# Kernel optimization log

Hardware: AMD Instinct MI355X
Metric: run time of the kernel (lower is better)

The kernel has to match this reference:

```python
import jax, jax.numpy as jnp
import numpy as np

# footprints from the module: RB = 8-neighbor ring (center excluded), G = 4-neighbor cross
RB_OFFSETS = [(-1, -1), (-1, 0), (-1, 1), (0, -1), (0, 1), (1, -1), (1, 0), (1, 1)]
G_OFFSETS = [(-1, 0), (0, -1), (0, 1), (1, 0)]
N_ITER = 3


def _footprint_median(x, offsets):
    """scipy.ndimage.median_filter with a boolean footprint.
    scipy uses rank = n//2 of the sorted footprint values (no averaging for even n)
    and 'reflect' boundary mode (== numpy 'symmetric' padding).
    x: [B, H, W]
    """
    B, H, W = x.shape
    xp = jnp.pad(x, ((0, 0), (1, 1), (1, 1)), mode='symmetric')
    vals = jnp.stack([xp[:, 1 + dy:1 + dy + H, 1 + dx:1 + dx + W]
                      for dy, dx in offsets], axis=0)  # [n, B, H, W]
    n = len(offsets)
    return jnp.sort(vals, axis=0)[n // 2]


def _conv3(x, k):
    """3x3 conv with symmetric padding. x: [B,H,W], k: [3,3] -> [B,H,W]."""
    xp = jnp.pad(x, ((0, 0), (1, 1), (1, 1)), mode='symmetric')[:, None]  # [B,1,H+2,W+2]
    kern = k[None, None].astype(x.dtype)  # [1,1,3,3]
    out = jax.lax.conv_general_dilated(xp, kern, (1, 1), 'VALID')
    return out[:, 0]


def _demosaick(x):
    """Naive bilinear demosaick of a GRBG Bayer mosaic. x: [B,H,W] -> [B,3,H,W]."""
    B, H, W = x.shape
    yy, xx = jnp.meshgrid(jnp.arange(H), jnp.arange(W), indexing='ij')
    r_mask = ((yy % 2 == 0) & (xx % 2 == 1)).astype(x.dtype)
    b_mask = ((yy % 2 == 1) & (xx % 2 == 0)).astype(x.dtype)
    g_mask = 1.0 - r_mask - b_mask
    KG = jnp.array([[0., 1., 0.], [1., 4., 1.], [0., 1., 0.]]) / 4.0
    KRB = jnp.array([[1., 2., 1.], [2., 4., 2.], [1., 2., 1.]]) / 4.0
    R = _conv3(x * r_mask, KRB)
    G = _conv3(x * g_mask, KG)
    Bc = _conv3(x * b_mask, KRB)
    return jnp.stack([R, G, Bc], axis=1)


def reference(image):
    # image: [B, 1, H, W] Bayer mosaic
    d = _demosaick(image[:, 0])  # [B, 3, H, W]
    R, G, B = d[:, 0], d[:, 1], d[:, 2]
    for _ in range(N_ITER):
        # medians are non-differentiable in the original (numpy roundtrip)
        R = jax.lax.stop_gradient(_footprint_median(R - G, RB_OFFSETS)) + G
        B = jax.lax.stop_gradient(_footprint_median(B - G, RB_OFFSETS)) + G
        G = 0.5 * (jax.lax.stop_gradient(_footprint_median(G - R, G_OFFSETS))
                   + jax.lax.stop_gradient(_footprint_median(G - B, G_OFFSETS))
                   + R + B)
    return jnp.stack([R, G, B], axis=1)


def setup_inputs() -> dict:
    key = jax.random.key(0)
    image = jax.random.uniform(key, (8, 1, 1024, 1024), dtype=jnp.float32)
    return {"image": image}
```

## Files before the change

kernel.cpp:

```cpp
#include <hip/hip_runtime.h>

#define HH 1024
#define WW 1024
#define NB 8
constexpr int PLANE = HH * WW;

#define S   84
#define RG  46
#define NTHR 512

typedef _Float16 h2 __attribute__((ext_vector_type(2)));

__device__ __forceinline__ int clampi(int v, int lo, int hi) {
    return v < lo ? lo : (v > hi ? hi : v);
}

union U2H { unsigned u; h2 h; };
__device__ __forceinline__ h2 u2h(unsigned v) { U2H x; x.u = v; return x.h; }
__device__ __forceinline__ unsigned h2u(h2 h) { U2H x; x.h = h; return x.u; }
__device__ __forceinline__ unsigned packdiff(float a, float b) {
    h2 h; h.x = (_Float16)a; h.y = (_Float16)b; return h2u(h);
}
__device__ __forceinline__ h2 swap16(h2 x) {
    unsigned u = h2u(x);
    return u2h(__builtin_amdgcn_alignbit(u, u, 16));
}

__device__ __forceinline__ void cswap2(h2& a, h2& b) {
    h2 lo = __builtin_elementwise_min(a, b);
    b = __builtin_elementwise_max(a, b);
    a = lo;
}

__device__ __forceinline__ h2 med8p(h2 v0, h2 v1, h2 v2, h2 v3,
                                    h2 v4, h2 v5, h2 v6, h2 v7) {
    cswap2(v0, v1); cswap2(v2, v3); cswap2(v4, v5); cswap2(v6, v7);
    cswap2(v0, v2); cswap2(v1, v3); cswap2(v4, v6); cswap2(v5, v7);
    cswap2(v1, v2); cswap2(v5, v6);
    h2 p2 = __builtin_elementwise_min(v2, v6), p3 = __builtin_elementwise_min(v3, v7);
    h2 p4 = __builtin_elementwise_max(v0, v4), p5 = __builtin_elementwise_max(v1, v5);
    return __builtin_elementwise_max(__builtin_elementwise_min(p3, p5),
                                     __builtin_elementwise_max(p2, p4));
}

__device__ __forceinline__ h2 med4p(h2 a, h2 b, h2 c, h2 d) {
    h2 ab_hi = __builtin_elementwise_max(a, b), ab_lo = __builtin_elementwise_min(a, b);
    h2 cd_hi = __builtin_elementwise_max(c, d), cd_lo = __builtin_elementwise_min(c, d);
    return __builtin_elementwise_max(__builtin_elementwise_min(ab_hi, cd_hi),
                                     __builtin_elementwise_max(ab_lo, cd_lo));
}

__device__ __forceinline__ void demo_acc(float v, int pyn, int pxn, int ady, int adx,
                                         float& accR, float& accG, float& accB) {
    bool isr = (pyn == 0) && (pxn == 1);
    bool isb = (pyn == 1) && (pxn == 0);
    float wrb = 0.25f * (float)((2 - ady) * (2 - adx));
    int man = ady + adx;
    float wg = (man == 0) ? 1.0f : ((man == 1) ? 0.25f : 0.0f);
    accR += isr ? wrb * v : 0.0f;
    accB += isb ? wrb * v : 0.0f;
    accG += (!isr && !isb) ? wg * v : 0.0f;
}

template <int CA>
__device__ __forceinline__ void load4u(const unsigned* row, int c0, unsigned w[4]) {
    if constexpr (CA == 0) {
        uint4 q = *reinterpret_cast<const uint4*>(row + c0);
        w[0] = q.x; w[1] = q.y; w[2] = q.z; w[3] = q.w;
    } else {
        uint2 a = *reinterpret_cast<const uint2*>(row + c0);
        uint2 b = *reinterpret_cast<const uint2*>(row + c0 + 2);
        w[0] = a.x; w[1] = a.y; w[2] = b.x; w[3] = b.y;
    }
}
template <int CA>
__device__ __forceinline__ void load6u(const unsigned* row, int c0, unsigned w[6]) {
    if constexpr (CA == 0) {
        uint4 q = *reinterpret_cast<const uint4*>(row + c0);
        w[0] = row[c0 - 1];
        w[1] = q.x; w[2] = q.y; w[3] = q.z; w[4] = q.w;
        w[5] = row[c0 + 4];
    } else {
        uint4 a = *reinterpret_cast<const uint4*>(row + c0 - 2);
        uint4 b = *reinterpret_cast<const uint4*>(row + c0 + 2);
        w[0] = a.y; w[1] = a.z; w[2] = a.w; w[3] = b.x; w[4] = b.y; w[5] = b.z;
    }
}
template <int CA>
__device__ __forceinline__ void store4u(unsigned* row, int c0, const unsigned v[4]) {
    if constexpr (CA == 0) {
        *reinterpret_cast<uint4*>(row + c0) = make_uint4(v[0], v[1], v[2], v[3]);
    } else {
        *reinterpret_cast<uint2*>(row + c0) = make_uint2(v[0], v[1]);
        *reinterpret_cast<uint2*>(row + c0 + 2) = make_uint2(v[2], v[3]);
    }
}

template <int R0, int NRP, int C0, int NG>
__device__ __forceinline__ void p1_int(const unsigned* __restrict__ sdRB,
                                       unsigned* __restrict__ uRB, int tid) {
    static_assert((C0 & 3) == 2, "p1_int needs C0 % 4 == 2");
    if (tid < NRP * NG) {
        int rp = tid / NG, g = tid - rp * NG;
        int r0 = R0 + 2 * rp;
        int c0 = C0 + 4 * g;
        int B = c0 - 2;
        unsigned w[4][6];
#pragma unroll
        for (int i = 0; i < 4; ++i) {
            const unsigned* row = &sdRB[(r0 - 1 + i) * S + B];
            uint4 q0 = *reinterpret_cast<const uint4*>(row);
            uint4 q1 = *reinterpret_cast<const uint4*>(row + 4);
            w[i][0] = q0.y; w[i][1] = q0.z; w[i][2] = q0.w;
            w[i][3] = q1.x; w[i][4] = q1.y; w[i][5] = q1.z;
        }
#pragma unroll
        for (int rr = 0; rr < 2; ++rr) {
            unsigned rv[4];
#pragma unroll
            for (int i = 0; i < 4; ++i) {
                h2 m = med8p(u2h(w[rr][i]), u2h(w[rr][i + 1]), u2h(w[rr][i + 2]),
                             u2h(w[rr + 1][i]), u2h(w[rr + 1][i + 2]),
                             u2h(w[rr + 2][i]), u2h(w[rr + 2][i + 1]), u2h(w[rr + 2][i + 2]));
                rv[i] = h2u(-m);
            }
            store4u<2>(&uRB[(r0 + rr) * S], c0, rv);
        }
    }
}

template <int R0, int NRP, int C0, int NG, int CA, bool FINAL>
__device__ __forceinline__ void p2_int(_Float16* __restrict__ sG, unsigned* __restrict__ sdRB,
                                       const unsigned* __restrict__ uRB, int tid,
                                       int y0, int x0,
                                       float* __restrict__ oR, float* __restrict__ oG,
                                       float* __restrict__ oB) {
    if (tid < NRP * NG) {
        int rp = tid / NG, g = tid - rp * NG;
        int r0 = R0 + 2 * rp;
        int c0 = C0 + 4 * g;
        unsigned wm[4], wp[4], w0[6], w1[6];
        load4u<CA>(&uRB[(r0 - 1) * S], c0, wm);
        load6u<CA>(&uRB[(r0) * S], c0, w0);
        load6u<CA>(&uRB[(r0 + 1) * S], c0, w1);
        load4u<CA>(&uRB[(r0 + 2) * S], c0, wp);
        h2 ga0 = *reinterpret_cast<const h2*>(&sG[r0 * S + c0]);
        h2 ga1 = *reinterpret_cast<const h2*>(&sG[r0 * S + c0 + 2]);
        h2 gb0 = *reinterpret_cast<const h2*>(&sG[(r0 + 1) * S + c0]);
        h2 gb1 = *reinterpret_cast<const h2*>(&sG[(r0 + 1) * S + c0 + 2]);
        _Float16 gr0[4] = {ga0.x, ga0.y, ga1.x, ga1.y};
        _Float16 gr1[4] = {gb0.x, gb0.y, gb1.x, gb1.y};
        const h2 half2v = {(_Float16)0.5f, (_Float16)0.5f};

        unsigned nd0[4], nd1[4];
        float R4[2][4], G4[2][4], B4[2][4];
#pragma unroll
        for (int i = 0; i < 4; ++i) {
            {
                h2 m = med4p(u2h(wm[i]), u2h(w0[i]), u2h(w0[i + 2]), u2h(w1[i + 1]));
                h2 uc = u2h(w0[i + 1]);
                h2 gg; gg.x = gr0[i]; gg.y = gr0[i];
                h2 RB = gg - uc;
                h2 Gn2 = ((m + swap16(m)) + (RB + swap16(RB))) * half2v;
                if constexpr (FINAL) {
                    R4[0][i] = (float)RB.x; B4[0][i] = (float)RB.y; G4[0][i] = (float)Gn2.x;
                } else {
                    nd0[i] = h2u(RB - Gn2);
                    gr0[i] = Gn2.x;
                }
            }
            {
                h2 m = med4p(u2h(w0[i + 1]), u2h(w1[i]), u2h(w1[i + 2]), u2h(wp[i]));
                h2 uc = u2h(w1[i + 1]);
                h2 gg; gg.x = gr1[i]; gg.y = gr1[i];
                h2 RB = gg - uc;
                h2 Gn2 = ((m + swap16(m)) + (RB + swap16(RB))) * half2v;
                if constexpr (FINAL) {
                    R4[1][i] = (float)RB.x; B4[1][i] = (float)RB.y; G4[1][i] = (float)Gn2.x;
                } else {
                    nd1[i] = h2u(RB - Gn2);
                    gr1[i] = Gn2.x;
                }
            }
        }
        if constexpr (FINAL) {
#pragma unroll
            for (int rr = 0; rr < 2; ++rr) {
                size_t o = (size_t)(y0 + r0 + rr) * WW + (x0 + c0);
                *reinterpret_cast<float4*>(&oR[o]) = make_float4(R4[rr][0], R4[rr][1], R4[rr][2], R4[rr][3]);
                *reinterpret_cast<float4*>(&oG[o]) = make_float4(G4[rr][0], G4[rr][1], G4[rr][2], G4[rr][3]);
                *reinterpret_cast<float4*>(&oB[o]) = make_float4(B4[rr][0], B4[rr][1], B4[rr][2], B4[rr][3]);
            }
        } else {
            h2 s00; s00.x = gr0[0]; s00.y = gr0[1];
            h2 s01; s01.x = gr0[2]; s01.y = gr0[3];
            h2 s10; s10.x = gr1[0]; s10.y = gr1[1];
            h2 s11; s11.x = gr1[2]; s11.y = gr1[3];
            *reinterpret_cast<h2*>(&sG[r0 * S + c0]) = s00;
            *reinterpret_cast<h2*>(&sG[r0 * S + c0 + 2]) = s01;
            *reinterpret_cast<h2*>(&sG[(r0 + 1) * S + c0]) = s10;
            *reinterpret_cast<h2*>(&sG[(r0 + 1) * S + c0 + 2]) = s11;
            store4u<CA>(&sdRB[r0 * S], c0, nd0);
            store4u<CA>(&sdRB[(r0 + 1) * S], c0, nd1);
        }
    }
}

__device__ void p1_b(const unsigned* sdRB, unsigned* uRB, int tid,
                     int y0, int x0, int rlo, int nr, int clo, int nc) {
    for (int t = tid; t < nr * nc; t += NTHR) {
        int r = rlo + t / nc, c = clo + t - (t / nc) * nc;
        int gy = clampi(y0 + r, 0, HH - 1), gx = clampi(x0 + c, 0, WW - 1);
        int rm = clampi(gy - 1, 0, HH - 1) - y0, rp = clampi(gy + 1, 0, HH - 1) - y0;
        int cm = clampi(gx - 1, 0, WW - 1) - x0, cp = clampi(gx + 1, 0, WW - 1) - x0;
        h2 m = med8p(u2h(sdRB[rm * S + cm]), u2h(sdRB[rm * S + c]), u2h(sdRB[rm * S + cp]),
                     u2h(sdRB[r * S + cm]), u2h(sdRB[r * S + cp]),
                     u2h(sdRB[rp * S + cm]), u2h(sdRB[rp * S + c]), u2h(sdRB[rp * S + cp]));
        uRB[r * S + c] = h2u(-m);
    }
}

__device__ void p2_b(_Float16* sG, unsigned* sdRB, const unsigned* uRB, int tid,
                     int y0, int x0, int rlo, int nr, int clo, int nc, bool fin,
                     float* oR, float* oG, float* oB) {
    for (int t = tid; t < nr * nc; t += NTHR) {
        int r = rlo + t / nc, c = clo + t - (t / nc) * nc;
        int gy = clampi(y0 + r, 0, HH - 1), gx = clampi(x0 + c, 0, WW - 1);
        int rm = clampi(gy - 1, 0, HH - 1) - y0, rp = clampi(gy + 1, 0, HH - 1) - y0;
        int cm = clampi(gx - 1, 0, WW - 1) - x0, cp = clampi(gx + 1, 0, WW - 1) - x0;
        h2 m = med4p(u2h(uRB[rm * S + c]), u2h(uRB[r * S + cm]),
                     u2h(uRB[r * S + cp]), u2h(uRB[rp * S + c]));
        h2 uc = u2h(uRB[r * S + c]);
        float Gc = (float)sG[r * S + c];
        float Rn = Gc - (float)uc.x, Bn = Gc - (float)uc.y;
        float Gn = 0.5f * ((float)m.x + (float)m.y + Rn + Bn);
        if (fin) {
            size_t o = (size_t)(y0 + r) * WW + (x0 + c);
            oR[o] = Rn; oG[o] = Gn; oB[o] = Bn;
        } else {
            sG[r * S + c] = (_Float16)Gn;
            sdRB[r * S + c] = packdiff(Rn - Gn, Bn - Gn);
        }
    }
}

__global__ __launch_bounds__(512, 8) void fused_kernel(const float* __restrict__ img,
                                                       float* __restrict__ dst) {
    __shared__ __align__(16) unsigned smem[9660];
    unsigned* uRB = smem;
    unsigned* sdRB = smem + RG * S;
    _Float16* sG = reinterpret_cast<_Float16*>(smem + 2 * RG * S);
    float* sI = reinterpret_cast<float*>(smem);

    int bx = blockIdx.x, by = blockIdx.y, bb = blockIdx.z;
    int x0 = bx * 64 - 8, y0 = by * 32 - 7;
    const float* im = img + (size_t)bb * PLANE;
    float* oR = dst + (size_t)bb * 3 * PLANE;
    float* oG = oR + PLANE;
    float* oB = oR + 2 * PLANE;
    int tid = threadIdx.x;
    bool interior = (bx >= 1 && bx <= 14 && by >= 1 && by <= 30);

    if (interior) {
        if (tid < 22 * 19) {
            int qi = tid / 19, g = tid - (tid / 19) * 19;
            int rA = 1 + 2 * qi;
            int B = 4 * g;
            const float* base = im + (size_t)(y0 + rA - 1) * WW + (x0 + B);
            float w[4][6];
#pragma unroll
            for (int i = 0; i < 4; ++i) {
                float4 a = *reinterpret_cast<const float4*>(base + (size_t)i * WW);
                float4 b = *reinterpret_cast<const float4*>(base + (size_t)i * WW + 4);
                w[i][0] = a.y; w[i][1] = a.z; w[i][2] = a.w;
                w[i][3] = b.x; w[i][4] = b.y; w[i][5] = b.z;
            }
#pragma unroll
            for (int q = 0; q < 2; ++q) {
                int jb = 1 + 2 * q;
                float g00 = w[1][jb];
                float r00 = 0.5f * (w[1][jb - 1] + w[1][jb + 1]);
                float b00 = 0.5f * (w[0][jb] + w[2][jb]);
                float r01 = w[1][jb + 1];
                float g01 = 0.25f * (w[0][jb + 1] + w[2][jb + 1] + w[1][jb] + w[1][jb + 2]);
                float b01 = 0.25f * (w[0][jb] + w[0][jb + 2] + w[2][jb] + w[2][jb + 2]);
                float b10 = w[2][jb];
                float g10 = 0.25f * (w[1][jb] + w[3][jb] + w[2][jb - 1] + w[2][jb + 1]);
                float r10 = 0.25f * (w[1][jb - 1] + w[1][jb + 1] + w[3][jb - 1] + w[3][jb + 1]);
                float g11 = w[2][jb + 1];
                float r11 = 0.5f * (w[1][jb + 1] + w[3][jb + 1]);
                float b11 = 0.5f * (w[2][jb] + w[2][jb + 2]);
                int a0 = rA * S + 2 + 4 * g + 2 * q;
                h2 gh0; gh0.x = (_Float16)g00; gh0.y = (_Float16)g01;
                h2 gh1; gh1.x = (_Float16)g10; gh1.y = (_Float16)g11;
                *reinterpret_cast<h2*>(&sG[a0]) = gh0;
                *reinterpret_cast<h2*>(&sG[a0 + S]) = gh1;
                *reinterpret_cast<uint2*>(&sdRB[a0]) =
                    make_uint2(packdiff(r00 - g00, b00 - g00), packdiff(r01 - g01, b01 - g01));
                *reinterpret_cast<uint2*>(&sdRB[a0 + S]) =
                    make_uint2(packdiff(r10 - g10, b10 - g10), packdiff(r11 - g11, b11 - g11));
            }
        }
        __syncthreads();
        p1_int<2, 21, 2, 19>(sdRB, uRB, tid);
        __syncthreads();
        p2_int<3, 20, 4, 18, 0, false>(sG, sdRB, uRB, tid, y0, x0, oR, oG, oB);
        __syncthreads();
        p1_int<4, 19, 2, 19>(sdRB, uRB, tid);
        __syncthreads();
        p2_int<5, 18, 6, 17, 2, false>(sG, sdRB, uRB, tid, y0, x0, oR, oG, oB);
        __syncthreads();
        p1_int<6, 17, 6, 17>(sdRB, uRB, tid);
        __syncthreads();
        p2_int<7, 16, 8, 16, 0, true>(sG, sdRB, uRB, tid, y0, x0, oR, oG, oB);
    } else {
        for (int t = tid; t < RG * S; t += NTHR) {
            int r = t / S, c = t - (t / S) * S;
            int gy = clampi(y0 + r, 0, HH - 1), gx = clampi(x0 + c, 0, WW - 1);
            sI[r * S + c] = im[(size_t)gy * WW + gx];
        }
        __syncthreads();
        {
            for (int t = tid; t < 44 * 76; t += NTHR) {
                int r = 1 + t / 76, c = 2 + t - (t / 76) * 76;
                int gy = clampi(y0 + r, 0, HH - 1), gx = clampi(x0 + c, 0, WW - 1);
                float accR = 0.f, accG = 0.f, accB = 0.f;
#pragma unroll
                for (int dy = -1; dy <= 1; ++dy)
#pragma unroll
                    for (int dx = -1; dx <= 1; ++dx) {
                        int cy = clampi(gy + dy, 0, HH - 1);
                        int cx = clampi(gx + dx, 0, WW - 1);
                        float v = sI[(cy - y0) * S + (cx - x0)];
                        demo_acc(v, cy & 1, cx & 1, dy < 0 ? -dy : dy, dx < 0 ? -dx : dx,
                                 accR, accG, accB);
                    }
                sG[r * S + c] = (_Float16)accG;
                sdRB[r * S + c] = packdiff(accR - accG, accB - accG);
            }
        }
        __syncthreads();
        p1_b(sdRB, uRB, tid, y0, x0, 2, 42, 3, 74);
        __syncthreads();
        p2_b(sG, sdRB, uRB, tid, y0, x0, 3, 40, 4, 72, false, oR, oG, oB);
        __syncthreads();
        p1_b(sdRB, uRB, tid, y0, x0, 4, 38, 5, 70);
        __syncthreads();
        p2_b(sG, sdRB, uRB, tid, y0, x0, 5, 36, 6, 68, false, oR, oG, oB);
        __syncthreads();
        p1_b(sdRB, uRB, tid, y0, x0, 6, 34, 7, 66);
        __syncthreads();
        p2_b(sG, sdRB, uRB, tid, y0, x0, 7, 32, 8, 64, true, oR, oG, oB);
    }
}

extern "C" void kernel_launch(void* const* d_in, const int* in_sizes, int n_in,
                              void* d_out, int out_size, void* d_ws, size_t ws_size,
                              hipStream_t stream) {
    const float* img = (const float*)d_in[0];
    float* out = (float*)d_out;
    dim3 block(NTHR);
    dim3 grid(16, 32, NB);
    fused_kernel<<<grid, block, 0, stream>>>(img, out);
}
```

Measured before the change: 136.3 us.

## Reuse vectorized interior paths for boundary tiles via halo refresh copies

Boundary tiles no longer use the scalar clamped-index median passes. They run the same templated vectorized p1_int/p2_int passes as interior tiles, with extra refresh steps that copy in-image values into out-of-image halo cells to emulate symmetric reflection. The demosaick for boundary tiles also uses the quad-vectorized path for the in-image core, falling back to the per-pixel clamped version only for the remaining edge pixels. This removes the divergence and slow path of edge blocks at the cost of extra sync barriers and correctness subtleties in the halo emulation. The p2_int final output writes for out-of-image cells also need care.

```diff
diff --git a/kernel.cpp b/kernel.cpp
--- a/kernel.cpp
+++ b/kernel.cpp
@@ -60,6 +60,35 @@
     accR += isr ? wrb * v : 0.0f;
     accB += isb ? wrb * v : 0.0f;
     accG += (!isr && !isb) ? wg * v : 0.0f;
+}
+
+__device__ __forceinline__ void demo_quads2(const float w[4][6], unsigned* __restrict__ sdRB,
+                                            _Float16* __restrict__ sG, int a0base) {
+#pragma unroll
+    for (int q = 0; q < 2; ++q) {
+        int jb = 1 + 2 * q;
+        float g00 = w[1][jb];
+        float r00 = 0.5f * (w[1][jb - 1] + w[1][jb + 1]);
+        float b00 = 0.5f * (w[0][jb] + w[2][jb]);
+        float r01 = w[1][jb + 1];
+        float g01 = 0.25f * (w[0][jb + 1] + w[2][jb + 1] + w[1][jb] + w[1][jb + 2]);
+        float b01 = 0.25f * (w[0][jb] + w[0][jb + 2] + w[2][jb] + w[2][jb + 2]);
+        float b10 = w[2][jb];
+        float g10 = 0.25f * (w[1][jb] + w[3][jb] + w[2][jb - 1] + w[2][jb + 1]);
+        float r10 = 0.25f * (w[1][jb - 1] + w[1][jb + 1] + w[3][jb - 1] + w[3][jb + 1]);
+        float g11 = w[2][jb + 1];
+        float r11 = 0.5f * (w[1][jb + 1] + w[3][jb + 1]);
+        float b11 = 0.5f * (w[2][jb] + w[2][jb + 2]);
+        int a0 = a0base + 2 * q;
+        h2 gh0; gh0.x = (_Float16)g00; gh0.y = (_Float16)g01;
+        h2 gh1; gh1.x = (_Float16)g10; gh1.y = (_Float16)g11;
+        *reinterpret_cast<h2*>(&sG[a0]) = gh0;
+        *reinterpret_cast<h2*>(&sG[a0 + S]) = gh1;
+        *reinterpret_cast<uint2*>(&sdRB[a0]) =
+            make_uint2(packdiff(r00 - g00, b00 - g00), packdiff(r01 - g01, b01 - g01));
+        *reinterpret_cast<uint2*>(&sdRB[a0 + S]) =
+            make_uint2(packdiff(r10 - g10, b10 - g10), packdiff(r11 - g11, b11 - g11));
+    }
 }
 
 template <int CA>
@@ -206,41 +235,27 @@
     }
 }
 
-__device__ void p1_b(const unsigned* sdRB, unsigned* uRB, int tid,
-                     int y0, int x0, int rlo, int nr, int clo, int nc) {
+__device__ __forceinline__ void refresh_d(unsigned* __restrict__ sdRB, _Float16* __restrict__ sG,
+                                          int tid, int y0, int x0,
+                                          int rlo, int nr, int clo, int nc) {
     for (int t = tid; t < nr * nc; t += NTHR) {
         int r = rlo + t / nc, c = clo + t - (t / nc) * nc;
-        int gy = clampi(y0 + r, 0, HH - 1), gx = clampi(x0 + c, 0, WW - 1);
-        int rm = clampi(gy - 1, 0, HH - 1) - y0, rp = clampi(gy + 1, 0, HH - 1) - y0;
-        int cm = clampi(gx - 1, 0, WW - 1) - x0, cp = clampi(gx + 1, 0, WW - 1) - x0;
-        h2 m = med8p(u2h(sdRB[rm * S + cm]), u2h(sdRB[rm * S + c]), u2h(sdRB[rm * S + cp]),
-                     u2h(sdRB[r * S + cm]), u2h(sdRB[r * S + cp]),
-                     u2h(sdRB[rp * S + cm]), u2h(sdRB[rp * S + c]), u2h(sdRB[rp * S + cp]));
-        uRB[r * S + c] = h2u(-m);
-    }
-}
-
-__device__ void p2_b(_Float16* sG, unsigned* sdRB, const unsigned* uRB, int tid,
-                     int y0, int x0, int rlo, int nr, int clo, int nc, bool fin,
-                     float* oR, float* oG, float* oB) {
+        int gy = y0 + r, gx = x0 + c;
+        if ((unsigned)gy < (unsigned)HH && (unsigned)gx < (unsigned)WW) continue;
+        int rs = clampi(gy, 0, HH - 1) - y0, cs = clampi(gx, 0, WW - 1) - x0;
+        sdRB[r * S + c] = sdRB[rs * S + cs];
+        sG[r * S + c] = sG[rs * S + cs];
+    }
+}
+__device__ __forceinline__ void refresh_u(unsigned* __restrict__ uRB,
+                                          int tid, int y0, int x0,
+                                          int rlo, int nr, int clo, int nc) {
     for (int t = tid; t < nr * nc; t += NTHR) {
         int r = rlo + t / nc, c = clo + t - (t / nc) * nc;
-        int gy = clampi(y0 + r, 0, HH - 1), gx = clampi(x0 + c, 0, WW - 1);
-        int rm = clampi(gy - 1, 0, HH - 1) - y0, rp = clampi(gy + 1, 0, HH - 1) - y0;
-        int cm = clampi(gx - 1, 0, WW - 1) - x0, cp = clampi(gx + 1, 0, WW - 1) - x0;
-        h2 m = med4p(u2h(uRB[rm * S + c]), u2h(uRB[r * S + cm]),
-                     u2h(uRB[r * S + cp]), u2h(uRB[rp * S + c]));
-        h2 uc = u2h(uRB[r * S + c]);
-        float Gc = (float)sG[r * S + c];
-        float Rn = Gc - (float)uc.x, Bn = Gc - (float)uc.y;
-        float Gn = 0.5f * ((float)m.x + (float)m.y + Rn + Bn);
-        if (fin) {
-            size_t o = (size_t)(y0 + r) * WW + (x0 + c);
-            oR[o] = Rn; oG[o] = Gn; oB[o] = Bn;
-        } else {
-            sG[r * S + c] = (_Float16)Gn;
-            sdRB[r * S + c] = packdiff(Rn - Gn, Bn - Gn);
-        }
+        int gy = y0 + r, gx = x0 + c;
+        if ((unsigned)gy < (unsigned)HH && (unsigned)gx < (unsigned)WW) continue;
+        int rs = clampi(gy, 0, HH - 1) - y0, cs = clampi(gx, 0, WW - 1) - x0;
+        uRB[r * S + c] = uRB[rs * S + cs];
     }
 }
 
@@ -275,31 +290,7 @@
                 w[i][0] = a.y; w[i][1] = a.z; w[i][2] = a.w;
                 w[i][3] = b.x; w[i][4] = b.y; w[i][5] = b.z;
             }
-#pragma unroll
-            for (int q = 0; q < 2; ++q) {
-                int jb = 1 + 2 * q;
-                float g00 = w[1][jb];
-                float r00 = 0.5f * (w[1][jb - 1] + w[1][jb + 1]);
-                float b00 = 0.5f * (w[0][jb] + w[2][jb]);
-                float r01 = w[1][jb + 1];
-                float g01 = 0.25f * (w[0][jb + 1] + w[2][jb + 1] + w[1][jb] + w[1][jb + 2]);
-                float b01 = 0.25f * (w[0][jb] + w[0][jb + 2] + w[2][jb] + w[2][jb + 2]);
-                float b10 = w[2][jb];
-                float g10 = 0.25f * (w[1][jb] + w[3][jb] + w[2][jb - 1] + w[2][jb + 1]);
-                float r10 = 0.25f * (w[1][jb - 1] + w[1][jb + 1] + w[3][jb - 1] + w[3][jb + 1]);
-                float g11 = w[2][jb + 1];
-                float r11 = 0.5f * (w[1][jb + 1] + w[3][jb + 1]);
-                float b11 = 0.5f * (w[2][jb] + w[2][jb + 2]);
-                int a0 = rA * S + 2 + 4 * g + 2 * q;
-                h2 gh0; gh0.x = (_Float16)g00; gh0.y = (_Float16)g01;
-                h2 gh1; gh1.x = (_Float16)g10; gh1.y = (_Float16)g11;
-                *reinterpret_cast<h2*>(&sG[a0]) = gh0;
-                *reinterpret_cast<h2*>(&sG[a0 + S]) = gh1;
-                *reinterpret_cast<uint2*>(&sdRB[a0]) =
-                    make_uint2(packdiff(r00 - g00, b00 - g00), packdiff(r01 - g01, b01 - g01));
-                *reinterpret_cast<uint2*>(&sdRB[a0 + S]) =
-                    make_uint2(packdiff(r10 - g10, b10 - g10), packdiff(r11 - g11, b11 - g11));
-            }
+            demo_quads2(w, sdRB, sG, rA * S + 2 + 4 * g);
         }
         __syncthreads();
         p1_int<2, 21, 2, 19>(sdRB, uRB, tid);
@@ -314,43 +305,83 @@
         __syncthreads();
         p2_int<7, 16, 8, 16, 0, true>(sG, sdRB, uRB, tid, y0, x0, oR, oG, oB);
     } else {
+        int rImgLo = (0 - y0) > 0 ? (0 - y0) : 0;
+        int rImgHi = (1023 - y0) < (RG - 1) ? (1023 - y0) : (RG - 1);
+        int cImgLo = (0 - x0) > 0 ? (0 - x0) : 0;
+        int cImgHi = (1023 - x0) < 79 ? (1023 - x0) : 79;
+        int raLo = rImgLo + 1; raLo += ((raLo & 1) ^ 1);
+        int raHi = rImgHi - 2; raHi -= ((raHi & 1) ^ 1);
+        if (raHi > 43) raHi = 43;
+        int gLo = (cImgLo + 3) >> 2;
+        int gHi = (cImgHi - 7) >> 2; if (gHi > 18) gHi = 18;
+        int vcLo = 2 + 4 * gLo, vcHi = 5 + 4 * gHi;
+        int nQr = (raHi - raLo) / 2 + 1;
+        int nG = gHi - gLo + 1;
+
         for (int t = tid; t < RG * S; t += NTHR) {
             int r = t / S, c = t - (t / S) * S;
             int gy = clampi(y0 + r, 0, HH - 1), gx = clampi(x0 + c, 0, WW - 1);
             sI[r * S + c] = im[(size_t)gy * WW + gx];
         }
         __syncthreads();
-        {
-            for (int t = tid; t < 44 * 76; t += NTHR) {
-                int r = 1 + t / 76, c = 2 + t - (t / 76) * 76;
-                int gy = clampi(y0 + r, 0, HH - 1), gx = clampi(x0 + c, 0, WW - 1);
-                float accR = 0.f, accG = 0.f, accB = 0.f;
-#pragma unroll
-                for (int dy = -1; dy <= 1; ++dy)
-#pragma unroll
-                    for (int dx = -1; dx <= 1; ++dx) {
-                        int cy = clampi(gy + dy, 0, HH - 1);
-                        int cx = clampi(gx + dx, 0, WW - 1);
-                        float v = sI[(cy - y0) * S + (cx - x0)];
-                        demo_acc(v, cy & 1, cx & 1, dy < 0 ? -dy : dy, dx < 0 ? -dx : dx,
-                                 accR, accG, accB);
-                    }
-                sG[r * S + c] = (_Float16)accG;
-                sdRB[r * S + c] = packdiff(accR - accG, accB - accG);
-            }
-        }
-        __syncthreads();
-        p1_b(sdRB, uRB, tid, y0, x0, 2, 42, 3, 74);
-        __syncthreads();
-        p2_b(sG, sdRB, uRB, tid, y0, x0, 3, 40, 4, 72, false, oR, oG, oB);
-        __syncthreads();
-        p1_b(sdRB, uRB, tid, y0, x0, 4, 38, 5, 70);
-        __syncthreads();
-        p2_b(sG, sdRB, uRB, tid, y0, x0, 5, 36, 6, 68, false, oR, oG, oB);
-        __syncthreads();
-        p1_b(sdRB, uRB, tid, y0, x0, 6, 34, 7, 66);
-        __syncthreads();
-        p2_b(sG, sdRB, uRB, tid, y0, x0, 7, 32, 8, 64, true, oR, oG, oB);
+        if (tid < nQr * nG) {
+            int qi = tid / nG, g = gLo + (tid - (tid / nG) * nG);
+            int rA = raLo + 2 * qi;
+            int B = 4 * g;
+            float w[4][6];
+#pragma unroll
+            for (int i = 0; i < 4; ++i) {
+                const float* row = &sI[(rA - 1 + i) * S + B];
+                float4 a = *reinterpret_cast<const float4*>(row);
+                float4 b = *reinterpret_cast<const float4*>(row + 4);
+                w[i][0] = a.y; w[i][1] = a.z; w[i][2] = a.w;
+                w[i][3] = b.x; w[i][4] = b.y; w[i][5] = b.z;
+            }
+            demo_quads2(w, sdRB, sG, rA * S + 2 + 4 * g);
+        }
+        for (int t = tid; t < 44 * 76; t += NTHR) {
+            int r = 1 + t / 76, c = 2 + t - (t / 76) * 76;
+            if (r < rImgLo || r > rImgHi || c < cImgLo || c > cImgHi) continue;
+            if (r >= raLo && r <= raHi + 1 && c >= vcLo && c <= vcHi) continue;
+            int gy = y0 + r, gx = x0 + c;
+            float accR = 0.f, accG = 0.f, accB = 0.f;
+#pragma unroll
+            for (int dy = -1; dy <= 1; ++dy)
+#pragma unroll
+                for (int dx = -1; dx <= 1; ++dx) {
+                    int cy = clampi(gy + dy, 0, HH - 1);
+                    int cx = clampi(gx + dx, 0, WW - 1);
+                    float v = sI[(cy - y0) * S + (cx - x0)];
+                    demo_acc(v, cy & 1, cx & 1, dy < 0 ? -dy : dy, dx < 0 ? -dx : dx,
+                             accR, accG, accB);
+                }
+            sG[r * S + c] = (_Float16)accG;
+            sdRB[r * S + c] = packdiff(accR - accG, accB - accG);
+        }
+        __syncthreads();
+        refresh_d(sdRB, sG, tid, y0, x0, 1, 44, 2, 76);
+        __syncthreads();
+        p1_int<2, 21, 2, 19>(sdRB, uRB, tid);
+        __syncthreads();
+        refresh_u(uRB, tid, y0, x0, 2, 42, 2, 76);
+        __syncthreads();
+        p2_int<3, 20, 4, 18, 0, false>(sG, sdRB, uRB, tid, y0, x0, oR, oG, oB);
+        __syncthreads();
+        refresh_d(sdRB, sG, tid, y0, x0, 3, 40, 4, 72);
+        __syncthreads();
+        p1_int<4, 19, 2, 19>(sdRB, uRB, tid);
+        __syncthreads();
+        refresh_u(uRB, tid, y0, x0, 4, 38, 2, 76);
+        __syncthreads();
+        p2_int<5, 18, 6, 17, 2, false>(sG, sdRB, uRB, tid, y0, x0, oR, oG, oB);
+        __syncthreads();
+        refresh_d(sdRB, sG, tid, y0, x0, 5, 36, 6, 68);
+        __syncthreads();
+        p1_int<6, 17, 6, 17>(sdRB, uRB, tid);
+        __syncthreads();
+        refresh_u(uRB, tid, y0, x0, 6, 34, 6, 68);
+        __syncthreads();
+        p2_int<7, 16, 8, 16, 0, true>(sG, sdRB, uRB, tid, y0, x0, oR, oG, oB);
     }
 }
 
```

Measured after the change: 155.7 us. 1.14x slower.
